# Kernel optimization log

Hardware: AMD Instinct MI355X
Metric: run time of the kernel (lower is better)

## Reference

```python
import jax, jax.numpy as jnp
import numpy as np
from scipy.optimize import linear_sum_assignment

B, N, K = 4, 100000, 16
EPS = 1e-6
W_CE, W_DICE = 2.0, 0.1


def setup_inputs() -> dict:
    key = jax.random.key(0)
    k1, k2, k3 = jax.random.split(key, 3)
    # predicted soft masks: probabilities over K object slots per point
    mask = jax.nn.softmax(jax.random.normal(k1, (B, N, K), dtype=jnp.float32), axis=-1)
    # ground-truth one-hot object masks
    labels = jax.random.randint(k2, (B, N), 0, K)
    gt_mask = jax.nn.one_hot(labels, K, dtype=jnp.float32)
    # per-point validity mask
    valid = (jax.random.uniform(k3, (B, N)) > 0.1).astype(jnp.float32)
    return {"mask": mask, "gt_mask": gt_mask, "valid": valid}


def _bce_terms(mask):
    m = jnp.clip(mask, EPS, 1.0 - EPS)
    return -jnp.log(m), -jnp.log1p(-m)  # cost when gt=1, cost when gt=0


def _match_cost_ce(mask, gt_mask, valid):
    # cost[b,i,j] = mean_n(valid) BCE(mask[:, :, i], gt_mask[:, :, j])
    # computed via einsum -- never materializes the (B,N,K,K) repeat of the torch code
    neg_log_m, neg_log_1m = _bce_terms(mask)
    v = valid[:, :, None]  # (B,N,1)
    pos = jnp.einsum('bni,bnj->bij', v * neg_log_m, gt_mask)
    neg = jnp.einsum('bni,bnj->bij', v * neg_log_1m, 1.0 - gt_mask)
    denom = jnp.maximum(jnp.sum(valid, axis=1), 1.0)[:, None, None]
    return (pos + neg) / denom  # (B,K,K)


def _match_cost_dice(mask, gt_mask, valid):
    v = valid[:, :, None]
    inter = jnp.einsum('bni,bnj->bij', v * mask, gt_mask)          # (B,K,K)
    sum_m = jnp.sum(v * mask, axis=1)[:, :, None]                   # (B,K,1)
    sum_g = jnp.sum(v * gt_mask, axis=1)[:, None, :]                # (B,1,K)
    return 1.0 - 2.0 * inter / (sum_m + sum_g + EPS)


def _match_mask_by_cost(cost):
    # faithful to the original: per-batch CPU Hungarian (scipy linear_sum_assignment)
    cost_np = np.asarray(jax.device_get(cost))
    n_object = cost_np.shape[-1]
    col = np.stack([linear_sum_assignment(cost_np[b], maximize=False)[1]
                    for b in range(cost_np.shape[0])], 0)
    perm = np.eye(n_object, dtype=np.float32)[col]  # (B,K,K)
    return jnp.asarray(perm)


def _ce_loss(mask, gt_mask, valid):
    neg_log_m, neg_log_1m = _bce_terms(mask)
    bce = gt_mask * neg_log_m + (1.0 - gt_mask) * neg_log_1m  # (B,N,K)
    v = valid[:, :, None]
    return jnp.sum(bce * v) / (jnp.maximum(jnp.sum(valid), 1.0) * mask.shape[-1])


def _dice_loss(mask, gt_mask, valid):
    v = valid[:, :, None]
    inter = jnp.sum(v * mask * gt_mask, axis=1)                     # (B,K)
    denom = jnp.sum(v * mask, axis=1) + jnp.sum(v * gt_mask, axis=1)
    return jnp.mean(1.0 - 2.0 * inter / (denom + EPS))


def reference(mask, gt_mask, valid):
    # 1) matching cost on detached predictions (gradients never flow through matching)
    m_det = jax.lax.stop_gradient(mask)
    cost = W_CE * _match_cost_ce(m_det, gt_mask, valid) \
         + W_DICE * _match_cost_dice(m_det, gt_mask, valid)
    # 2) Hungarian matching -> permutation (B,K,K)
    perm = _match_mask_by_cost(cost)
    # 3) permute gt slots, detach
    gt_perm = jax.lax.stop_gradient(jnp.einsum('bij,bnj->bni', perm, gt_mask))
    # 4) weighted CE + Dice loss
    l_ce = _ce_loss(mask, gt_perm, valid)
    l_dice = _dice_loss(mask, gt_perm, valid)
    loss = W_CE * l_ce + W_DICE * l_dice
    return loss
```

## Files before the change

kernel.cpp:

```cpp
#include <hip/hip_runtime.h>

#define NBATCH 4
#define NROWS  100000
#define KD     16
#define EPSF   1e-6f
#define WCE    2.0f
#define WDICE  0.1f
#define NREP   8
#define LN2F   0.6931471805599453f
#define SRS    272

typedef __attribute__((ext_vector_type(8))) short short8;
typedef __attribute__((ext_vector_type(4))) float f32x4;

__device__ __forceinline__ unsigned short bf16rne(float x) {
  unsigned u = __float_as_uint(x);
  unsigned r = u + 0x7FFFu + ((u >> 16) & 1u);
  return (unsigned short)(r >> 16);
}

__device__ __forceinline__ void async_copy16(const float* g, float* l) {
  __builtin_amdgcn_global_load_lds(
      (const __attribute__((address_space(1))) float*)g,
      (__attribute__((address_space(3))) float*)l, 16, 0, 0);
}

__global__ __launch_bounds__(256, 4) void sml_accum(
    const float* __restrict__ mask, const float* __restrict__ gt,
    const float* __restrict__ valid, float* __restrict__ ws)
{
  const int b    = blockIdx.y;
  const int tid  = (int)threadIdx.x;
  const int lane = tid & 63;
  const int wv   = tid >> 6;
  const int q    = lane >> 4;
  const int c    = lane & 15;
  const int row0 = blockIdx.x * 256;

  __shared__ float sBuf[9216];
  float* sM = sBuf;
  float* sG = sBuf + 16 * SRS;

  const float* maskb  = mask  + (size_t)b * NROWS * KD;
  const float* gtb    = gt    + (size_t)b * NROWS * KD;
  const float* validb = valid + (size_t)b * NROWS;

#pragma unroll
  for (int i = 0; i < 4; ++i) {
    const int g   = i * 256 + tid;
    const int rg  = row0 + (g >> 2);
    const int rc  = (rg < NROWS) ? rg : (NROWS - 1);
    const size_t off = (size_t)rc * KD + (size_t)(g & 3) * 4;
    const int dst = (g >> 6) * SRS + (g & 63) * 4;
    async_copy16(maskb + off, &sM[dst]);
    async_copy16(gtb   + off, &sG[dst]);
  }
  __syncthreads();

  f32x4 accP = {0.f, 0.f, 0.f, 0.f};
  f32x4 accQ = {0.f, 0.f, 0.f, 0.f};
  f32x4 accI = {0.f, 0.f, 0.f, 0.f};

#pragma unroll
  for (int ch = 0; ch < 2; ++ch) {
    const int rt = wv * 64 + ch * 32 + 8 * q;
    float m[8], g[8], vv[8];
#pragma unroll
    for (int t = 0; t < 8; ++t) {
      const int r = rt + t;
      const int a = (r >> 4) * SRS + (r & 15) * 16 + c;
      m[t] = sM[a];
      g[t] = sG[a];
    }
    const int grow = row0 + rt;
    if (grow + 7 < NROWS) {
      const float4 va = *(const float4*)(validb + grow);
      const float4 vb4 = *(const float4*)(validb + grow + 4);
      vv[0] = va.x; vv[1] = va.y; vv[2] = va.z; vv[3] = va.w;
      vv[4] = vb4.x; vv[5] = vb4.y; vv[6] = vb4.z; vv[7] = vb4.w;
    } else {
#pragma unroll
      for (int t = 0; t < 8; ++t)
        vv[t] = (grow + t < NROWS) ? validb[grow + t] : 0.f;
    }

    short8 fP, fQ, fI, fB;
#pragma unroll
    for (int t = 0; t < 8; ++t) {
      const float mc = fminf(fmaxf(m[t], EPSF), 1.f - EPSF);
      const float lm = __log2f(mc);
      const float l1 = __log2f(1.f - mc);
      fP[t] = (short)bf16rne(LN2F * (l1 - lm));
      fQ[t] = (short)bf16rne(-LN2F * l1);
      fI[t] = (short)bf16rne(m[t]);
      fB[t] = (short)bf16rne(vv[t] * g[t]);
    }
    accP = __builtin_amdgcn_mfma_f32_16x16x32_bf16(fP, fB, accP, 0, 0, 0);
    accQ = __builtin_amdgcn_mfma_f32_16x16x32_bf16(fQ, fB, accQ, 0, 0, 0);
    accI = __builtin_amdgcn_mfma_f32_16x16x32_bf16(fI, fB, accI, 0, 0, 0);
  }

  __syncthreads();
#pragma unroll
  for (int r = 0; r < 4; ++r) {
    const int idx = (4 * q + r) * 16 + c;
    sBuf[wv * 768 + idx]        = accP[r];
    sBuf[3072 + wv * 768 + idx] = accQ[r];
    sBuf[6144 + wv * 768 + idx] = accI[r];
  }
  __syncthreads();

  const int rep = blockIdx.x & (NREP - 1);
  float* wsb = ws + ((size_t)rep * NBATCH + b) * 768;
  {
    float sP = 0.f, sQ = 0.f, sI = 0.f;
#pragma unroll
    for (int wvv = 0; wvv < 4; ++wvv) {
      sP += sBuf[wvv * 768 + tid];
      sQ += sBuf[3072 + wvv * 768 + tid];
      sI += sBuf[6144 + wvv * 768 + tid];
    }
    unsafeAtomicAdd(&wsb[tid],       sP);
    unsafeAtomicAdd(&wsb[256 + tid], sQ);
    unsafeAtomicAdd(&wsb[512 + tid], sI);
  }
}

#define DPP_U(x, C) ((unsigned)__builtin_amdgcn_update_dpp(0, (int)(x), (C), 0xF, 0xF, true))

__device__ __forceinline__ float rowsum16(float x) {
  x += __uint_as_float(DPP_U(__float_as_uint(x), 0x128));
  x += __uint_as_float(DPP_U(__float_as_uint(x), 0x124));
  x += __uint_as_float(DPP_U(__float_as_uint(x), 0x122));
  x += __uint_as_float(DPP_U(__float_as_uint(x), 0x121));
  return x;
}
__device__ __forceinline__ unsigned rowmin16(unsigned x) {
  unsigned y;
  y = DPP_U(x, 0x128); x = (y < x) ? y : x;
  y = DPP_U(x, 0x124); x = (y < x) ? y : x;
  y = DPP_U(x, 0x122); x = (y < x) ? y : x;
  y = DPP_U(x, 0x121); x = (y < x) ? y : x;
  return x;
}
__device__ __forceinline__ float readlane_f(float x, int l) {
  return __int_as_float(__builtin_amdgcn_readlane(__float_as_int(x), l));
}
__device__ __forceinline__ int rfl(int x) { return __builtin_amdgcn_readfirstlane(x); }

__device__ __forceinline__ float sel16v(int idx,
  float x0, float x1, float x2, float x3, float x4, float x5, float x6, float x7,
  float x8, float x9, float x10, float x11, float x12, float x13, float x14, float x15)
{
  const float a0 = (idx & 1) ? x1  : x0;
  const float a1 = (idx & 1) ? x3  : x2;
  const float a2 = (idx & 1) ? x5  : x4;
  const float a3 = (idx & 1) ? x7  : x6;
  const float a4 = (idx & 1) ? x9  : x8;
  const float a5 = (idx & 1) ? x11 : x10;
  const float a6 = (idx & 1) ? x13 : x12;
  const float a7 = (idx & 1) ? x15 : x14;
  const float b0 = (idx & 2) ? a1 : a0;
  const float b1 = (idx & 2) ? a3 : a2;
  const float b2 = (idx & 2) ? a5 : a4;
  const float b3 = (idx & 2) ? a7 : a6;
  const float c0 = (idx & 4) ? b1 : b0;
  const float c1 = (idx & 4) ? b3 : b2;
  return (idx & 8) ? c1 : c0;
}

#define R16(M) M(0) M(1) M(2) M(3) M(4) M(5) M(6) M(7) M(8) M(9) M(10) M(11) M(12) M(13) M(14) M(15)
#define SEL16(p, idx) sel16v(idx, p##0,p##1,p##2,p##3,p##4,p##5,p##6,p##7,p##8,p##9,p##10,p##11,p##12,p##13,p##14,p##15)

#define LD3(i)  const float pc##i = sB[i*16 + col]; \
                const float qc##i = sB[256 + i*16 + col]; \
                const float ic##i = sB[512 + i*16 + col];
#define SGQS(i) sg += ic##i; qs += qc##i;
#define MKA(i)  const float Sm##i = rowsum16(ic##i); \
  const float a##i = WCE * (pc##i + rowsum16(qc##i)) / Vb \
                   + WDICE * (1.f - 2.f * ic##i / (Sm##i + sg + EPSF));
#define PKA(i)  const unsigned t##i = (__float_as_uint(a##i + 64.f) & 0xFFFFFFF0u) | (unsigned)i;

__global__ __launch_bounds__(256, 1) void sml_solve(const float* __restrict__ ws,
                                                    float* __restrict__ out)
{
  const int tid = (int)threadIdx.x;
  const int w   = tid >> 6;
  const int l   = tid & 63;
  const int col = l & 15;
  __shared__ float sAcc[NBATCH][768];
  __shared__ float part[NBATCH][3];

  float* sB = sAcc[w];
#pragma unroll
  for (int k = 0; k < 3; ++k) {
    const int idx4 = k * 64 + l;
    float4 s = {0.f, 0.f, 0.f, 0.f};
#pragma unroll
    for (int r = 0; r < NREP; ++r) {
      const float4 t = *(const float4*)(ws + ((size_t)r * NBATCH + w) * 768 + idx4 * 4);
      s.x += t.x; s.y += t.y; s.z += t.z; s.w += t.w;
    }
    *(float4*)&sB[idx4 * 4] = s;
  }
  __syncthreads();

  R16(LD3)
  float sg = 0.f, qs = 0.f;
  R16(SGQS)
  const float V    = rowsum16(sg);
  const float Vb   = fmaxf(V, 1.f);
  const float Btot = rowsum16(qs);
  R16(MKA)

  R16(PKA)
  unsigned mA, mB2, mC2, mD2;
  {
    const unsigned s0 = t0  < t1  ? t0  : t1;
    const unsigned s1 = t2  < t3  ? t2  : t3;
    const unsigned s2 = t4  < t5  ? t4  : t5;
    const unsigned s3 = t6  < t7  ? t6  : t7;
    const unsigned s4 = t8  < t9  ? t8  : t9;
    const unsigned s5 = t10 < t11 ? t10 : t11;
    const unsigned s6 = t12 < t13 ? t12 : t13;
    const unsigned s7 = t14 < t15 ? t14 : t15;
    mA  = s0 < s1 ? s0 : s1;
    mB2 = s2 < s3 ? s2 : s3;
    mC2 = s4 < s5 ? s4 : s5;
    mD2 = s6 < s7 ? s6 : s7;
  }
  const unsigned mAB = mA < mB2 ? mA : mB2;
  const unsigned mCD = mC2 < mD2 ? mC2 : mD2;
  const unsigned mall = mAB < mCD ? mAB : mCD;
  const int r0i = (int)(mall & 15u);
  float vdual = SEL16(a, r0i);

  unsigned long long pword = 0ull;
  unsigned pmask = 0u;
  unsigned rowused = 0u;
#pragma unroll
  for (int j = 0; j < 16; ++j) {
    const int rj = __builtin_amdgcn_readlane(r0i, j);
    if (!((rowused >> rj) & 1u)) {
      rowused |= 1u << rj;
      pmask   |= 1u << j;
      pword   |= (unsigned long long)rj << (4 * j);
    }
  }

  float u_t = 0.f;

  for (int i = 0; i < 16; ++i) {
    if ((rowused >> i) & 1u) continue;
    float minv = 1e30f;
    int   way  = -1;
    bool  used = false;
    float Dent = 0.f;
    float Dcum = 0.f;
    bool  intree = (col == i);
    int   i0 = i;
    int   j0 = -1;

    for (int it = 0; it < 17; ++it) {
      const float u0  = readlane_f(u_t, i0);
      const float cur = SEL16(a, i0) - u0 - vdual;
      if (!used && cur < minv) { minv = cur; way = j0; }
      unsigned pk = (__float_as_uint((used ? 1e30f : minv) + 64.f) & 0xFFFFFFF0u)
                  | (unsigned)col;
      pk = rowmin16(pk);
      const float delta = __uint_as_float(pk & 0xFFFFFFF0u) - 64.f;
      if (used) vdual -= delta; else minv -= delta;
      Dcum += delta;
      const int j1s = rfl((int)(pk & 15u));
      const int  pj1 = rfl((int)((pword >> (4 * j1s)) & 15ull));
      const bool asg = (pmask >> j1s) & 1u;
      j0 = j1s;
      if (!asg) break;
      used   = used   || (col == j1s);
      Dent   = (col == pj1) ? Dcum : Dent;
      intree = intree || (col == pj1);
      i0 = pj1;
    }
    u_t += intree ? (Dcum - Dent) : 0.f;

    int jcur = rfl(j0);
    for (int s = 0; s < 17; ++s) {
      const int wy   = rfl(__builtin_amdgcn_readlane(way, jcur));
      const int prev = (wy >= 0) ? (int)((pword >> (4 * wy)) & 15ull) : i;
      pword = (pword & ~(15ull << (4 * jcur)))
            | ((unsigned long long)prev << (4 * jcur));
      pmask |= 1u << jcur;
      if (wy < 0) break;
      jcur = rfl(wy);
    }
  }

  const int ri  = (int)((pword >> (4 * col)) & 15ull);
  const float pcm = SEL16(pc, ri);
  const float icm = SEL16(ic, ri);
  const float smv = SEL16(Sm, ri);
  const float cce = rowsum16(pcm);
  const float dce = rowsum16(1.f - 2.f * icm / (smv + sg + EPSF));
  if (l == 0) { part[w][0] = cce + Btot; part[w][1] = dce; part[w][2] = V; }
  __syncthreads();

  if (tid == 0) {
    float C = 0.f, D = 0.f, Vt = 0.f;
#pragma unroll
    for (int bb = 0; bb < NBATCH; ++bb) {
      C += part[bb][0]; D += part[bb][1]; Vt += part[bb][2];
    }
    Vt = fmaxf(Vt, 1.f);
    out[0] = WCE * C / (Vt * (float)KD) + WDICE * D / 64.f;
  }
}

extern "C" void kernel_launch(void* const* d_in, const int* in_sizes, int n_in,
                              void* d_out, int out_size, void* d_ws, size_t ws_size,
                              hipStream_t stream)
{
  (void)in_sizes; (void)n_in; (void)out_size; (void)ws_size;
  const float* mask  = (const float*)d_in[0];
  const float* gt    = (const float*)d_in[1];
  const float* valid = (const float*)d_in[2];
  float* out = (float*)d_out;
  float* ws  = (float*)d_ws;

  hipMemsetAsync(d_ws, 0, (size_t)NREP * NBATCH * 768 * sizeof(float), stream);

  dim3 grid((NROWS + 255) / 256, NBATCH);
  sml_accum<<<grid, 256, 0, stream>>>(mask, gt, valid, ws);
  sml_solve<<<1, 256, 0, stream>>>(ws, out);
}
```

Baseline: 103.9 us.

## Double-buffer async LDS tiles in accumulate kernel and add auction warm-start to solver

The accumulate kernel now processes four 256-row tiles per block, using double-buffered LDS and prefetching the next tile with async global-to-LDS copies while the current tile is computed. The grid shrinks to 98 blocks per batch and launch bounds drop to 2 waves per SIMD. This reduces the number of atomic flushes and overlaps load latency with MFMA work. The Hungarian solver also gains a bounded auction-style warm-start phase that assigns rows before the exact augmenting-path loop, aiming to cut the number of serial iterations. In exchange, the accumulate grid has fewer blocks and uses more LDS per block, which may lower occupancy.

```diff
diff --git a/kernel.cpp b/kernel.cpp
--- a/kernel.cpp
+++ b/kernel.cpp
@@ -9,6 +9,8 @@
 #define NREP   8
 #define LN2F   0.6931471805599453f
 #define SRS    272
+#define TILES  4
+#define GX     98
 
 typedef __attribute__((ext_vector_type(8))) short short8;
 typedef __attribute__((ext_vector_type(4))) float f32x4;
@@ -25,7 +27,7 @@
       (__attribute__((address_space(3))) float*)l, 16, 0, 0);
 }
 
-__global__ __launch_bounds__(256, 4) void sml_accum(
+__global__ __launch_bounds__(256, 2) void sml_accum(
     const float* __restrict__ mask, const float* __restrict__ gt,
     const float* __restrict__ valid, float* __restrict__ ws)
 {
@@ -35,69 +37,85 @@
   const int wv   = tid >> 6;
   const int q    = lane >> 4;
   const int c    = lane & 15;
-  const int row0 = blockIdx.x * 256;
-
-  __shared__ float sBuf[9216];
-  float* sM = sBuf;
-  float* sG = sBuf + 16 * SRS;
+  const int bx   = (int)blockIdx.x;
+
+  __shared__ float sBuf[17408];
 
   const float* maskb  = mask  + (size_t)b * NROWS * KD;
   const float* gtb    = gt    + (size_t)b * NROWS * KD;
   const float* validb = valid + (size_t)b * NROWS;
 
+  f32x4 accP = {0.f, 0.f, 0.f, 0.f};
+  f32x4 accQ = {0.f, 0.f, 0.f, 0.f};
+  f32x4 accI = {0.f, 0.f, 0.f, 0.f};
+
 #pragma unroll
   for (int i = 0; i < 4; ++i) {
     const int g   = i * 256 + tid;
-    const int rg  = row0 + (g >> 2);
+    const int rg  = bx * 1024 + (g >> 2);
     const int rc  = (rg < NROWS) ? rg : (NROWS - 1);
     const size_t off = (size_t)rc * KD + (size_t)(g & 3) * 4;
     const int dst = (g >> 6) * SRS + (g & 63) * 4;
-    async_copy16(maskb + off, &sM[dst]);
-    async_copy16(gtb   + off, &sG[dst]);
-  }
-  __syncthreads();
-
-  f32x4 accP = {0.f, 0.f, 0.f, 0.f};
-  f32x4 accQ = {0.f, 0.f, 0.f, 0.f};
-  f32x4 accI = {0.f, 0.f, 0.f, 0.f};
-
-#pragma unroll
-  for (int ch = 0; ch < 2; ++ch) {
-    const int rt = wv * 64 + ch * 32 + 8 * q;
-    float m[8], g[8], vv[8];
-#pragma unroll
-    for (int t = 0; t < 8; ++t) {
-      const int r = rt + t;
-      const int a = (r >> 4) * SRS + (r & 15) * 16 + c;
-      m[t] = sM[a];
-      g[t] = sG[a];
-    }
-    const int grow = row0 + rt;
-    if (grow + 7 < NROWS) {
-      const float4 va = *(const float4*)(validb + grow);
-      const float4 vb4 = *(const float4*)(validb + grow + 4);
-      vv[0] = va.x; vv[1] = va.y; vv[2] = va.z; vv[3] = va.w;
-      vv[4] = vb4.x; vv[5] = vb4.y; vv[6] = vb4.z; vv[7] = vb4.w;
-    } else {
-#pragma unroll
-      for (int t = 0; t < 8; ++t)
-        vv[t] = (grow + t < NROWS) ? validb[grow + t] : 0.f;
-    }
-
-    short8 fP, fQ, fI, fB;
-#pragma unroll
-    for (int t = 0; t < 8; ++t) {
-      const float mc = fminf(fmaxf(m[t], EPSF), 1.f - EPSF);
-      const float lm = __log2f(mc);
-      const float l1 = __log2f(1.f - mc);
-      fP[t] = (short)bf16rne(LN2F * (l1 - lm));
-      fQ[t] = (short)bf16rne(-LN2F * l1);
-      fI[t] = (short)bf16rne(m[t]);
-      fB[t] = (short)bf16rne(vv[t] * g[t]);
-    }
-    accP = __builtin_amdgcn_mfma_f32_16x16x32_bf16(fP, fB, accP, 0, 0, 0);
-    accQ = __builtin_amdgcn_mfma_f32_16x16x32_bf16(fQ, fB, accQ, 0, 0, 0);
-    accI = __builtin_amdgcn_mfma_f32_16x16x32_bf16(fI, fB, accI, 0, 0, 0);
+    async_copy16(maskb + off, &sBuf[dst]);
+    async_copy16(gtb   + off, &sBuf[dst + 4352]);
+  }
+
+  for (int t = 0; t < TILES; ++t) {
+    __syncthreads();
+    const int base = (t & 1) * 8704;
+
+    if (t + 1 < TILES) {
+      const int nb = ((t + 1) & 1) * 8704;
+#pragma unroll
+      for (int i = 0; i < 4; ++i) {
+        const int g   = i * 256 + tid;
+        const int rg  = bx * 1024 + (t + 1) * 256 + (g >> 2);
+        const int rc  = (rg < NROWS) ? rg : (NROWS - 1);
+        const size_t off = (size_t)rc * KD + (size_t)(g & 3) * 4;
+        const int dst = nb + (g >> 6) * SRS + (g & 63) * 4;
+        async_copy16(maskb + off, &sBuf[dst]);
+        async_copy16(gtb   + off, &sBuf[dst + 4352]);
+      }
+    }
+
+#pragma unroll
+    for (int ch = 0; ch < 2; ++ch) {
+      const int rt = wv * 64 + ch * 32 + 8 * q;
+      float m[8], g[8], vv[8];
+#pragma unroll
+      for (int tt = 0; tt < 8; ++tt) {
+        const int r = rt + tt;
+        const int a = base + (r >> 4) * SRS + (r & 15) * 16 + c;
+        m[tt] = sBuf[a];
+        g[tt] = sBuf[a + 4352];
+      }
+      const int grow = bx * 1024 + t * 256 + rt;
+      if (grow + 7 < NROWS) {
+        const float4 va  = *(const float4*)(validb + grow);
+        const float4 vb4 = *(const float4*)(validb + grow + 4);
+        vv[0] = va.x; vv[1] = va.y; vv[2] = va.z; vv[3] = va.w;
+        vv[4] = vb4.x; vv[5] = vb4.y; vv[6] = vb4.z; vv[7] = vb4.w;
+      } else {
+#pragma unroll
+        for (int tt = 0; tt < 8; ++tt)
+          vv[tt] = (grow + tt < NROWS) ? validb[grow + tt] : 0.f;
+      }
+
+      short8 fP, fQ, fI, fB;
+#pragma unroll
+      for (int tt = 0; tt < 8; ++tt) {
+        const float mc = fminf(fmaxf(m[tt], EPSF), 1.f - EPSF);
+        const float lm = __log2f(mc);
+        const float l1 = __log2f(1.f - mc);
+        fP[tt] = (short)bf16rne(LN2F * (l1 - lm));
+        fQ[tt] = (short)bf16rne(-LN2F * l1);
+        fI[tt] = (short)bf16rne(m[tt]);
+        fB[tt] = (short)bf16rne(vv[tt] * g[tt]);
+      }
+      accP = __builtin_amdgcn_mfma_f32_16x16x32_bf16(fP, fB, accP, 0, 0, 0);
+      accQ = __builtin_amdgcn_mfma_f32_16x16x32_bf16(fQ, fB, accQ, 0, 0, 0);
+      accI = __builtin_amdgcn_mfma_f32_16x16x32_bf16(fI, fB, accI, 0, 0, 0);
+    }
   }
 
   __syncthreads();
@@ -110,7 +128,7 @@
   }
   __syncthreads();
 
-  const int rep = blockIdx.x & (NREP - 1);
+  const int rep = bx & (NREP - 1);
   float* wsb = ws + ((size_t)rep * NBATCH + b) * 768;
   {
     float sP = 0.f, sQ = 0.f, sI = 0.f;
@@ -250,6 +268,43 @@
 
   float u_t = 0.f;
 
+  {
+    int steps = 24;
+    for (int i = 0; i < 16 && steps > 0; ++i) {
+      if ((rowused >> i) & 1u) continue;
+      int icur = i;
+      while (steps-- > 0) {
+        const float d = SEL16(a, icur) - vdual;
+        unsigned pk1 = (__float_as_uint(d + 64.f) & 0xFFFFFFF0u) | (unsigned)col;
+        const unsigned m1 = rowmin16(pk1);
+        const int j1 = rfl((int)(m1 & 15u));
+        const unsigned pk2 = (col == j1) ? 0xFFFFFFFFu : pk1;
+        const unsigned m2 = rowmin16(pk2);
+        const int j2 = rfl((int)(m2 & 15u));
+        const float d1 = readlane_f(d, j1);
+        const float d2 = readlane_f(d, j2);
+        const bool strict = d1 < d2;
+        int jt = j1;
+        if (strict) {
+          if (col == j1) vdual -= (d2 - d1);
+        } else {
+          const bool occ1 = (pmask >> j1) & 1u;
+          const bool occ2 = (pmask >> j2) & 1u;
+          if (occ1 && !occ2) jt = j2;
+        }
+        if (col == icur) u_t = d2;
+        const bool occ = (pmask >> jt) & 1u;
+        const int owner = occ ? (int)((pword >> (4 * jt)) & 15ull) : -1;
+        pword = (pword & ~(15ull << (4 * jt)))
+              | ((unsigned long long)icur << (4 * jt));
+        pmask   |= 1u << jt;
+        rowused |= 1u << icur;
+        if (owner >= 0) { rowused &= ~(1u << owner); icur = owner; }
+        else break;
+      }
+    }
+  }
+
   for (int i = 0; i < 16; ++i) {
     if ((rowused >> i) & 1u) continue;
     float minv = 1e30f;
@@ -328,7 +383,7 @@
 
   hipMemsetAsync(d_ws, 0, (size_t)NREP * NBATCH * 768 * sizeof(float), stream);
 
-  dim3 grid((NROWS + 255) / 256, NBATCH);
+  dim3 grid(GX, NBATCH);
   sml_accum<<<grid, 256, 0, stream>>>(mask, gt, valid, ws);
   sml_solve<<<1, 256, 0, stream>>>(ws, out);
 }
```

Result: slower. 111.1 us (+7.0%).

## Fuse accumulation and Hungarian solve into one kernel via last-block counter

Applied to the files above, without the earlier changes.

Merges the accumulation kernel and the single-block solve kernel into one launch. Each block bumps a global counter after its atomics, and the last block to finish reads the reduced workspace with coherent loads and runs the matching and loss. This removes one kernel launch and the gap between the two kernels. In exchange it adds a threadfence and a counter atomic to every block, and the solve now runs in a block launched with the heavier 4-blocks-per-CU bound, which may limit its registers.

```diff
diff --git a/kernel.cpp b/kernel.cpp
--- a/kernel.cpp
+++ b/kernel.cpp
@@ -9,6 +9,8 @@
 #define NREP   8
 #define LN2F   0.6931471805599453f
 #define SRS    272
+#define GXR    391
+#define NBLK   (GXR * NBATCH)
 
 typedef __attribute__((ext_vector_type(8))) short short8;
 typedef __attribute__((ext_vector_type(4))) float f32x4;
@@ -25,105 +27,8 @@
       (__attribute__((address_space(3))) float*)l, 16, 0, 0);
 }
 
-__global__ __launch_bounds__(256, 4) void sml_accum(
-    const float* __restrict__ mask, const float* __restrict__ gt,
-    const float* __restrict__ valid, float* __restrict__ ws)
-{
-  const int b    = blockIdx.y;
-  const int tid  = (int)threadIdx.x;
-  const int lane = tid & 63;
-  const int wv   = tid >> 6;
-  const int q    = lane >> 4;
-  const int c    = lane & 15;
-  const int row0 = blockIdx.x * 256;
-
-  __shared__ float sBuf[9216];
-  float* sM = sBuf;
-  float* sG = sBuf + 16 * SRS;
-
-  const float* maskb  = mask  + (size_t)b * NROWS * KD;
-  const float* gtb    = gt    + (size_t)b * NROWS * KD;
-  const float* validb = valid + (size_t)b * NROWS;
-
-#pragma unroll
-  for (int i = 0; i < 4; ++i) {
-    const int g   = i * 256 + tid;
-    const int rg  = row0 + (g >> 2);
-    const int rc  = (rg < NROWS) ? rg : (NROWS - 1);
-    const size_t off = (size_t)rc * KD + (size_t)(g & 3) * 4;
-    const int dst = (g >> 6) * SRS + (g & 63) * 4;
-    async_copy16(maskb + off, &sM[dst]);
-    async_copy16(gtb   + off, &sG[dst]);
-  }
-  __syncthreads();
-
-  f32x4 accP = {0.f, 0.f, 0.f, 0.f};
-  f32x4 accQ = {0.f, 0.f, 0.f, 0.f};
-  f32x4 accI = {0.f, 0.f, 0.f, 0.f};
-
-#pragma unroll
-  for (int ch = 0; ch < 2; ++ch) {
-    const int rt = wv * 64 + ch * 32 + 8 * q;
-    float m[8], g[8], vv[8];
-#pragma unroll
-    for (int t = 0; t < 8; ++t) {
-      const int r = rt + t;
-      const int a = (r >> 4) * SRS + (r & 15) * 16 + c;
-      m[t] = sM[a];
-      g[t] = sG[a];
-    }
-    const int grow = row0 + rt;
-    if (grow + 7 < NROWS) {
-      const float4 va = *(const float4*)(validb + grow);
-      const float4 vb4 = *(const float4*)(validb + grow + 4);
-      vv[0] = va.x; vv[1] = va.y; vv[2] = va.z; vv[3] = va.w;
-      vv[4] = vb4.x; vv[5] = vb4.y; vv[6] = vb4.z; vv[7] = vb4.w;
-    } else {
-#pragma unroll
-      for (int t = 0; t < 8; ++t)
-        vv[t] = (grow + t < NROWS) ? validb[grow + t] : 0.f;
-    }
-
-    short8 fP, fQ, fI, fB;
-#pragma unroll
-    for (int t = 0; t < 8; ++t) {
-      const float mc = fminf(fmaxf(m[t], EPSF), 1.f - EPSF);
-      const float lm = __log2f(mc);
-      const float l1 = __log2f(1.f - mc);
-      fP[t] = (short)bf16rne(LN2F * (l1 - lm));
-      fQ[t] = (short)bf16rne(-LN2F * l1);
-      fI[t] = (short)bf16rne(m[t]);
-      fB[t] = (short)bf16rne(vv[t] * g[t]);
-    }
-    accP = __builtin_amdgcn_mfma_f32_16x16x32_bf16(fP, fB, accP, 0, 0, 0);
-    accQ = __builtin_amdgcn_mfma_f32_16x16x32_bf16(fQ, fB, accQ, 0, 0, 0);
-    accI = __builtin_amdgcn_mfma_f32_16x16x32_bf16(fI, fB, accI, 0, 0, 0);
-  }
-
-  __syncthreads();
-#pragma unroll
-  for (int r = 0; r < 4; ++r) {
-    const int idx = (4 * q + r) * 16 + c;
-    sBuf[wv * 768 + idx]        = accP[r];
-    sBuf[3072 + wv * 768 + idx] = accQ[r];
-    sBuf[6144 + wv * 768 + idx] = accI[r];
-  }
-  __syncthreads();
-
-  const int rep = blockIdx.x & (NREP - 1);
-  float* wsb = ws + ((size_t)rep * NBATCH + b) * 768;
-  {
-    float sP = 0.f, sQ = 0.f, sI = 0.f;
-#pragma unroll
-    for (int wvv = 0; wvv < 4; ++wvv) {
-      sP += sBuf[wvv * 768 + tid];
-      sQ += sBuf[3072 + wvv * 768 + tid];
-      sI += sBuf[6144 + wvv * 768 + tid];
-    }
-    unsafeAtomicAdd(&wsb[tid],       sP);
-    unsafeAtomicAdd(&wsb[256 + tid], sQ);
-    unsafeAtomicAdd(&wsb[512 + tid], sI);
-  }
+__device__ __forceinline__ float gload_coh(const float* p) {
+  return __hip_atomic_load(p, __ATOMIC_RELAXED, __HIP_MEMORY_SCOPE_AGENT);
 }
 
 #define DPP_U(x, C) ((unsigned)__builtin_amdgcn_update_dpp(0, (int)(x), (C), 0xF, 0xF, true))
@@ -177,34 +82,142 @@
                 const float ic##i = sB[512 + i*16 + col];
 #define SGQS(i) sg += ic##i; qs += qc##i;
 #define MKA(i)  const float Sm##i = rowsum16(ic##i); \
-  const float a##i = WCE * (pc##i + rowsum16(qc##i)) / Vb \
-                   + WDICE * (1.f - 2.f * ic##i / (Sm##i + sg + EPSF));
-#define PKA(i)  const unsigned t##i = (__float_as_uint(a##i + 64.f) & 0xFFFFFFF0u) | (unsigned)i;
-
-__global__ __launch_bounds__(256, 1) void sml_solve(const float* __restrict__ ws,
-                                                    float* __restrict__ out)
+  const float aa##i = WCE * (pc##i + rowsum16(qc##i)) / Vb \
+                    + WDICE * (1.f - 2.f * ic##i / (Sm##i + sg + EPSF));
+#define PKA(i)  const unsigned t##i = (__float_as_uint(aa##i + 64.f) & 0xFFFFFFF0u) | (unsigned)i;
+
+__global__ __launch_bounds__(256, 4) void sml_fused(
+    const float* __restrict__ mask, const float* __restrict__ gt,
+    const float* __restrict__ valid, float* __restrict__ ws,
+    float* __restrict__ out)
 {
-  const int tid = (int)threadIdx.x;
-  const int w   = tid >> 6;
+  const int b    = blockIdx.y;
+  const int tid  = (int)threadIdx.x;
+  const int lane = tid & 63;
+  const int wv   = tid >> 6;
+  const int q    = lane >> 4;
+  const int c    = lane & 15;
+  const int row0 = blockIdx.x * 256;
+
+  __shared__ float sBuf[9216];
+  __shared__ float partS[NBATCH][3];
+  __shared__ int   isLast;
+  float* sM = sBuf;
+  float* sG = sBuf + 16 * SRS;
+
+  const float* maskb  = mask  + (size_t)b * NROWS * KD;
+  const float* gtb    = gt    + (size_t)b * NROWS * KD;
+  const float* validb = valid + (size_t)b * NROWS;
+
+#pragma unroll
+  for (int i = 0; i < 4; ++i) {
+    const int g   = i * 256 + tid;
+    const int rg  = row0 + (g >> 2);
+    const int rc  = (rg < NROWS) ? rg : (NROWS - 1);
+    const size_t off = (size_t)rc * KD + (size_t)(g & 3) * 4;
+    const int dst = (g >> 6) * SRS + (g & 63) * 4;
+    async_copy16(maskb + off, &sM[dst]);
+    async_copy16(gtb   + off, &sG[dst]);
+  }
+  __syncthreads();
+
+  f32x4 accP = {0.f, 0.f, 0.f, 0.f};
+  f32x4 accQ = {0.f, 0.f, 0.f, 0.f};
+  f32x4 accI = {0.f, 0.f, 0.f, 0.f};
+
+#pragma unroll
+  for (int ch = 0; ch < 2; ++ch) {
+    const int rt = wv * 64 + ch * 32 + 8 * q;
+    float m[8], g[8], vv[8];
+#pragma unroll
+    for (int t = 0; t < 8; ++t) {
+      const int r = rt + t;
+      const int a = (r >> 4) * SRS + (r & 15) * 16 + c;
+      m[t] = sM[a];
+      g[t] = sG[a];
+    }
+    const int grow = row0 + rt;
+    if (grow + 7 < NROWS) {
+      const float4 va  = *(const float4*)(validb + grow);
+      const float4 vb4 = *(const float4*)(validb + grow + 4);
+      vv[0] = va.x; vv[1] = va.y; vv[2] = va.z; vv[3] = va.w;
+      vv[4] = vb4.x; vv[5] = vb4.y; vv[6] = vb4.z; vv[7] = vb4.w;
+    } else {
+#pragma unroll
+      for (int t = 0; t < 8; ++t)
+        vv[t] = (grow + t < NROWS) ? validb[grow + t] : 0.f;
+    }
+
+    short8 fP, fQ, fI, fB;
+#pragma unroll
+    for (int t = 0; t < 8; ++t) {
+      const float mc = fminf(fmaxf(m[t], EPSF), 1.f - EPSF);
+      const float lm = __log2f(mc);
+      const float l1 = __log2f(1.f - mc);
+      fP[t] = (short)bf16rne(LN2F * (l1 - lm));
+      fQ[t] = (short)bf16rne(-LN2F * l1);
+      fI[t] = (short)bf16rne(m[t]);
+      fB[t] = (short)bf16rne(vv[t] * g[t]);
+    }
+    accP = __builtin_amdgcn_mfma_f32_16x16x32_bf16(fP, fB, accP, 0, 0, 0);
+    accQ = __builtin_amdgcn_mfma_f32_16x16x32_bf16(fQ, fB, accQ, 0, 0, 0);
+    accI = __builtin_amdgcn_mfma_f32_16x16x32_bf16(fI, fB, accI, 0, 0, 0);
+  }
+
+  __syncthreads();
+#pragma unroll
+  for (int r = 0; r < 4; ++r) {
+    const int idx = (4 * q + r) * 16 + c;
+    sBuf[wv * 768 + idx]        = accP[r];
+    sBuf[3072 + wv * 768 + idx] = accQ[r];
+    sBuf[6144 + wv * 768 + idx] = accI[r];
+  }
+  __syncthreads();
+
+  const int rep = (int)blockIdx.x & (NREP - 1);
+  float* wsb = ws + ((size_t)rep * NBATCH + b) * 768;
+  {
+    float sP = 0.f, sQ = 0.f, sI = 0.f;
+#pragma unroll
+    for (int wvv = 0; wvv < 4; ++wvv) {
+      sP += sBuf[wvv * 768 + tid];
+      sQ += sBuf[3072 + wvv * 768 + tid];
+      sI += sBuf[6144 + wvv * 768 + tid];
+    }
+    unsafeAtomicAdd(&wsb[tid],       sP);
+    unsafeAtomicAdd(&wsb[256 + tid], sQ);
+    unsafeAtomicAdd(&wsb[512 + tid], sI);
+  }
+
+  __threadfence();
+  __syncthreads();
+  if (tid == 0) {
+    const unsigned old = atomicAdd((unsigned*)(ws + NREP * NBATCH * 768), 1u);
+    isLast = (old == (unsigned)(NBLK - 1));
+  }
+  __syncthreads();
+  if (!isLast) return;
+  __threadfence();
+
+  const int w2  = tid >> 6;
   const int l   = tid & 63;
   const int col = l & 15;
-  __shared__ float sAcc[NBATCH][768];
-  __shared__ float part[NBATCH][3];
-
-  float* sB = sAcc[w];
-#pragma unroll
-  for (int k = 0; k < 3; ++k) {
-    const int idx4 = k * 64 + l;
-    float4 s = {0.f, 0.f, 0.f, 0.f};
-#pragma unroll
+
+  {
+    float acc[12];
+#pragma unroll
+    for (int k = 0; k < 12; ++k) acc[k] = 0.f;
     for (int r = 0; r < NREP; ++r) {
-      const float4 t = *(const float4*)(ws + ((size_t)r * NBATCH + w) * 768 + idx4 * 4);
-      s.x += t.x; s.y += t.y; s.z += t.z; s.w += t.w;
-    }
-    *(float4*)&sB[idx4 * 4] = s;
-  }
-  __syncthreads();
-
+      const float* base = ws + ((size_t)r * NBATCH + w2) * 768;
+#pragma unroll
+      for (int k = 0; k < 12; ++k) acc[k] += gload_coh(base + k * 64 + l);
+    }
+#pragma unroll
+    for (int k = 0; k < 12; ++k) sBuf[w2 * 768 + k * 64 + l] = acc[k];
+  }
+  __syncthreads();
+
+  const float* sB = sBuf + w2 * 768;
   R16(LD3)
   float sg = 0.f, qs = 0.f;
   R16(SGQS)
@@ -229,11 +242,11 @@
     mC2 = s4 < s5 ? s4 : s5;
     mD2 = s6 < s7 ? s6 : s7;
   }
-  const unsigned mAB = mA < mB2 ? mA : mB2;
-  const unsigned mCD = mC2 < mD2 ? mC2 : mD2;
+  const unsigned mAB  = mA  < mB2 ? mA  : mB2;
+  const unsigned mCD  = mC2 < mD2 ? mC2 : mD2;
   const unsigned mall = mAB < mCD ? mAB : mCD;
   const int r0i = (int)(mall & 15u);
-  float vdual = SEL16(a, r0i);
+  float vdual = SEL16(aa, r0i);
 
   unsigned long long pword = 0ull;
   unsigned pmask = 0u;
@@ -263,7 +276,7 @@
 
     for (int it = 0; it < 17; ++it) {
       const float u0  = readlane_f(u_t, i0);
-      const float cur = SEL16(a, i0) - u0 - vdual;
+      const float cur = SEL16(aa, i0) - u0 - vdual;
       if (!used && cur < minv) { minv = cur; way = j0; }
       unsigned pk = (__float_as_uint((used ? 1e30f : minv) + 64.f) & 0xFFFFFFF0u)
                   | (unsigned)col;
@@ -301,14 +314,14 @@
   const float smv = SEL16(Sm, ri);
   const float cce = rowsum16(pcm);
   const float dce = rowsum16(1.f - 2.f * icm / (smv + sg + EPSF));
-  if (l == 0) { part[w][0] = cce + Btot; part[w][1] = dce; part[w][2] = V; }
+  if (l == 0) { partS[w2][0] = cce + Btot; partS[w2][1] = dce; partS[w2][2] = V; }
   __syncthreads();
 
   if (tid == 0) {
     float C = 0.f, D = 0.f, Vt = 0.f;
 #pragma unroll
     for (int bb = 0; bb < NBATCH; ++bb) {
-      C += part[bb][0]; D += part[bb][1]; Vt += part[bb][2];
+      C += partS[bb][0]; D += partS[bb][1]; Vt += partS[bb][2];
     }
     Vt = fmaxf(Vt, 1.f);
     out[0] = WCE * C / (Vt * (float)KD) + WDICE * D / 64.f;
@@ -326,9 +339,8 @@
   float* out = (float*)d_out;
   float* ws  = (float*)d_ws;
 
-  hipMemsetAsync(d_ws, 0, (size_t)NREP * NBATCH * 768 * sizeof(float), stream);
-
-  dim3 grid((NROWS + 255) / 256, NBATCH);
-  sml_accum<<<grid, 256, 0, stream>>>(mask, gt, valid, ws);
-  sml_solve<<<1, 256, 0, stream>>>(ws, out);
-}
+  hipMemsetAsync(d_ws, 0, (size_t)(NREP * NBATCH * 768 + 1) * sizeof(float), stream);
+
+  dim3 grid(GXR, NBATCH);
+  sml_fused<<<grid, 256, 0, stream>>>(mask, gt, valid, ws, out);
+}
```

Measured after the change: 204.3 us. +96.7%, slower.
